# Performance work log

Hardware: AMD Instinct MI355X
Metric: run time of the kernel (lower is better)

Reference implementation:

```python
import jax, jax.numpy as jnp
import numpy as np

EPS = 1e-6  # T5LayerNorm epsilon


def setup_inputs() -> dict:
    key = jax.random.key(0)
    k0, k1, k2, k3 = jax.random.split(key, 4)
    B, S, D, F, E = 4, 2048, 768, 3072, 8
    hidden_states = jax.random.normal(k0, (B, S, D), jnp.float32)
    router_w = jax.random.normal(k1, (E, D), jnp.float32) * 0.02
    ln_w = jnp.ones((E, D), jnp.float32)
    wi = jax.random.normal(k2, (E, F, D), jnp.float32) * 0.02
    wo = jax.random.normal(k3, (E, D, F), jnp.float32) * 0.02
    return {"hidden_states": hidden_states, "router_w": router_w, "ln_w": ln_w,
            "wi": wi, "wo": wo, "top_k": 2}


def reference(hidden_states, router_w, ln_w, wi, wo, top_k):
    B, S, D = hidden_states.shape
    E = router_w.shape[0]
    x = hidden_states.reshape(-1, D)                      # [T, D] tokens
    router_logits = x @ router_w.T                        # [T, E]
    probs = jax.nn.softmax(router_logits, axis=-1)
    rw, sel = jax.lax.top_k(probs, top_k)                 # [T, K]
    rw = rw / jnp.sum(rw, axis=-1, keepdims=True)         # renormalize top-k weights

    # T5LayerNorm is RMS-norm (no mean subtraction); shared input x, per-expert scale.
    var = jnp.mean(x * x, axis=-1, keepdims=True)         # [T, 1]
    x_norm = x * jax.lax.rsqrt(var + EPS)                 # [T, D]

    out = jnp.zeros_like(x)
    for e in range(E):  # fixed small loop over experts (structurally distinct params)
        # combine weight for expert e: zero for tokens that did not select it
        w_e = jnp.sum(jnp.where(sel == e, rw, 0.0), axis=-1)   # [T]
        h = x_norm * ln_w[e]                                   # [T, D]
        ff = jax.nn.relu(h @ wi[e].T) @ wo[e].T                # [T, D]
        # T5LayerFF returns x + FFN(LN(x)); routing weight scales the whole output
        out = out + w_e[:, None] * (x + ff)
    layer_output = out.reshape(B, S, D)
    return layer_output, router_logits
```

## Files before the change

### kernel.cpp

```cpp
#include <hip/hip_runtime.h>
#include <hip/hip_bf16.h>
#include <math.h>

typedef short short8 __attribute__((ext_vector_type(8)));
typedef float f32x16 __attribute__((ext_vector_type(16)));

constexpr int D = 768;
constexpr int E = 8;
constexpr int F = 3072;
constexpr int FH = 1536;
constexpr int T = 8192;
constexpr float EPS = 1e-6f;

static __device__ inline unsigned short f2bf(float f) {
    __hip_bfloat16 h = __float2bfloat16(f);
    return *reinterpret_cast<unsigned short*>(&h);
}

static __device__ inline f32x16 mfma_bf16(short8 a, short8 b, f32x16 c) {
    return __builtin_amdgcn_mfma_f32_32x32x16_bf16(a, b, c, 0, 0, 0);
}

#define GLL16(g, s) __builtin_amdgcn_global_load_lds( \
    (const __attribute__((address_space(1))) unsigned int*)(g), \
    (__attribute__((address_space(3))) unsigned int*)(s), 16, 0, 0)

__global__ __launch_bounds__(256)
void convert_weights(const float* __restrict__ wi, const float* __restrict__ wo,
                     const float* __restrict__ lnw,
                     unsigned short* __restrict__ wip, unsigned short* __restrict__ wop)
{
    const unsigned NWI = (unsigned)E * F * D;
    unsigned i4 = (blockIdx.x * 256u + threadIdx.x) * 4u;
    if (i4 < NWI) {
        float4 v = *(const float4*)(wi + i4);
        unsigned e = i4 / (unsigned)(F * D);
        unsigned d = i4 % (unsigned)D;
        float4 l = *(const float4*)(lnw + e * D + d);
        ushort4 o = { f2bf(v.x * l.x), f2bf(v.y * l.y), f2bf(v.z * l.z), f2bf(v.w * l.w) };
        *(ushort4*)(wip + i4) = o;
    } else {
        unsigned j = i4 - NWI;
        float4 v = *(const float4*)(wo + j);
        ushort4 o = { f2bf(v.x), f2bf(v.y), f2bf(v.z), f2bf(v.w) };
        *(ushort4*)(wop + j) = o;
    }
}

__global__ __launch_bounds__(256)
void router_norm_kernel(const float* __restrict__ x,
                        const float* __restrict__ rw,
                        float* __restrict__ logits,
                        unsigned short* __restrict__ xn,
                        float* __restrict__ out,
                        int*   __restrict__ sel,
                        float2* __restrict__ w01)
{
    const int lane = threadIdx.x & 63;
    const int wid  = threadIdx.x >> 6;
    const int t = blockIdx.x * 4 + wid;
    if (t >= T) return;

    const float* xr = x + (size_t)t * D;
    float xv[12];
    float acc[8];
#pragma unroll
    for (int e = 0; e < 8; ++e) acc[e] = 0.f;
    float ssq = 0.f;
#pragma unroll
    for (int i = 0; i < 12; ++i) {
        const int k = lane + 64 * i;
        const float v = xr[k];
        xv[i] = v;
        ssq += v * v;
#pragma unroll
        for (int e = 0; e < 8; ++e) acc[e] += v * rw[e * D + k];
    }
#pragma unroll
    for (int off = 32; off; off >>= 1) {
        ssq += __shfl_xor(ssq, off);
#pragma unroll
        for (int e = 0; e < 8; ++e) acc[e] += __shfl_xor(acc[e], off);
    }

    int e0 = 0; float m0 = acc[0];
#pragma unroll
    for (int e = 1; e < 8; ++e) if (acc[e] > m0) { m0 = acc[e]; e0 = e; }
    int e1 = -1; float m1 = -3.4e38f;
#pragma unroll
    for (int e = 0; e < 8; ++e) if (e != e0 && acc[e] > m1) { m1 = acc[e]; e1 = e; }

    const float r  = expf(m1 - m0);
    const float w0 = 1.f / (1.f + r);
    const float w1 = r * w0;
    const float wsum = w0 + w1;
    const float rs = rsqrtf(ssq * (1.f / (float)D) + EPS);

    if (lane == 0) {
#pragma unroll
        for (int e = 0; e < 8; ++e) logits[t * 8 + e] = acc[e];
        sel[t] = e0 | (e1 << 4);
        w01[t] = make_float2(w0, w1);
    }

#pragma unroll
    for (int i = 0; i < 12; ++i) {
        const int k = lane + 64 * i;
        xn[(size_t)t * D + k] = f2bf(xv[i] * rs);
        out[(size_t)t * D + k] = wsum * xv[i];
    }
}

__global__ __launch_bounds__(256)
void build_lists(const int* __restrict__ sel, const float2* __restrict__ w01,
                 int* __restrict__ counts, int* __restrict__ lists,
                 float* __restrict__ wlist)
{
    const int e = blockIdx.x;
    const int tid = threadIdx.x;
    const int lane = tid & 63;
    const int wv = tid >> 6;
    __shared__ int wtot[4];
    int cnt = 0;
    for (int c0 = 0; c0 < T; c0 += 256) {
        const int t = c0 + tid;
        const int s = sel[t];
        const bool m1 = ((s >> 4) & 15) == e;
        const bool m = ((s & 15) == e) || m1;
        const unsigned long long b = __ballot(m);
        const int pre = __popcll(b & ((1ULL << lane) - 1ULL));
        if (lane == 0) wtot[wv] = __popcll(b);
        __syncthreads();
        int wbase = 0;
#pragma unroll
        for (int i = 0; i < 4; ++i) if (i < wv) wbase += wtot[i];
        if (m) {
            const int pos = cnt + wbase + pre;
            lists[e * T + pos] = (t << 1) | (m1 ? 1 : 0);
            const float2 w = w01[t];
            wlist[e * T + pos] = m1 ? w.y : w.x;
        }
        cnt += wtot[0] + wtot[1] + wtot[2] + wtot[3];
        __syncthreads();
    }
    if (tid == 0) counts[e] = cnt;
}


#define GEMM_PIPE_LOOP(NKT)                                                   \
           \
    _Pragma("unroll")                                                         \
    for (int j = 0; j < 4; ++j) {                                             \
        GLL16(aSrc[j], smem + stg + j * 1024);                                \
        GLL16(bSrc[j], smem + 16384 + stg + j * 1024);                        \
    }                                                                         \
    _Pragma("unroll")                                                         \
    for (int j = 0; j < 4; ++j) {                                             \
        GLL16(aSrc[j] + 64, smem + 32768 + stg + j * 1024);                   \
        GLL16(bSrc[j] + 64, smem + 32768 + 16384 + stg + j * 1024);           \
    }                                                                         \
    asm volatile("s_waitcnt vmcnt(8)" ::: "memory");                          \
    __builtin_amdgcn_s_barrier();                                             \
    int cur = 0;                                                              \
    for (int kt = 0; kt < (NKT); ++kt) {                                      \
        const char* cA = smem + cur * 32768;                                  \
        const char* cB = cA + 16384;                                          \
        short8 fA0[4], fA1[4], fB0[4], fB1[4];                                \
        _Pragma("unroll")                                                     \
        for (int ks = 0; ks < 4; ++ks) {                                      \
            const int coff = (hi * 16 + ks * 32) ^ rx;                        \
            fA0[ks] = *(const short8*)(cA + arow0 + coff);                    \
            fA1[ks] = *(const short8*)(cA + arow1 + coff);                    \
            fB0[ks] = *(const short8*)(cB + brow0 + coff);                    \
            fB1[ks] = *(const short8*)(cB + brow1 + coff);                    \
        }                                                                     \
        asm volatile("s_waitcnt lgkmcnt(0)" ::: "memory");                    \
        __builtin_amdgcn_sched_barrier(0);                                    \
        __builtin_amdgcn_s_barrier();    \
        {                                                                     \
            const int kn = (kt + 2 < (NKT) ? kt + 2 : (NKT)-1) * 64;          \
            char* dA = smem + cur * 32768;                                    \
            _Pragma("unroll")                                                 \
            for (int j = 0; j < 4; ++j) {                                     \
                GLL16(aSrc[j] + kn, dA + stg + j * 1024);                     \
                GLL16(bSrc[j] + kn, dA + 16384 + stg + j * 1024);             \
            }                                                                 \
        }                                                                     \
        __builtin_amdgcn_sched_barrier(0);                                    \
        _Pragma("unroll")                                                     \
        for (int ks = 0; ks < 4; ++ks) {                                      \
            acc00 = mfma_bf16(fA0[ks], fB0[ks], acc00);                       \
            acc01 = mfma_bf16(fA0[ks], fB1[ks], acc01);                       \
            acc10 = mfma_bf16(fA1[ks], fB0[ks], acc10);                       \
            acc11 = mfma_bf16(fA1[ks], fB1[ks], acc11);                       \
        }                                                                     \
        asm volatile("s_waitcnt vmcnt(8)" ::: "memory");                      \
        __builtin_amdgcn_s_barrier();    \
        cur ^= 1;                                                             \
    }

__global__ __launch_bounds__(256)
void gemm1_kernel(const unsigned short* __restrict__ xn,
                  const unsigned short* __restrict__ wip,
                  const int* __restrict__ counts,
                  const int* __restrict__ lists,
                  unsigned short* __restrict__ H, int half)
{
    __shared__ __align__(16) char smem[65536];
    __shared__ int s_tok[128];

    const int bid = blockIdx.x;
    const int e  = bid & 7;
    const int mt = (bid >> 3) / 12;
    const int nt = (bid >> 3) % 12;
    const int cnt = counts[e];
    const int base = mt * 128;
    if (base >= cnt) return;
    int offe = 0;
    for (int i = 0; i < e; ++i) offe += counts[i];

    const int tid = threadIdx.x;
    const int w = tid >> 6, l = tid & 63;
    const int lo = l & 31, hi = l >> 5;
    const int wr = w >> 1, wc = w & 1;

    if (tid < 128) {
        const int idx = base + tid;
        s_tok[tid] = (idx < cnt) ? (lists[e * T + idx] >> 1) : 0;
    }
    __syncthreads();

    const int r = (w * 4 + 0) * 8 + (l >> 3);
    const int chS = ((l & 7) ^ ((l >> 3) & 7)) * 8;
    const unsigned short* aSrc[4];
    const unsigned short* bSrc[4];
#pragma unroll
    for (int j = 0; j < 4; ++j) {
        const int rj = r + j * 8;
        aSrc[j] = xn + (size_t)s_tok[rj] * D + chS;
        bSrc[j] = wip + ((size_t)e * F + half * FH + nt * 128 + rj) * D + chS;
    }

    f32x16 acc00, acc01, acc10, acc11;
#pragma unroll
    for (int q = 0; q < 16; ++q) { acc00[q] = 0.f; acc01[q] = 0.f; acc10[q] = 0.f; acc11[q] = 0.f; }

    const int rx = (lo & 7) << 4;
    const int arow0 = (wr * 64 + lo) * 128;
    const int arow1 = arow0 + 32 * 128;
    const int brow0 = (wc * 64 + lo) * 128;
    const int brow1 = brow0 + 32 * 128;
    const int stg = w * 4096;

    GEMM_PIPE_LOOP(12)

    const int cbase = nt * 128 + wc * 64 + lo;
#pragma unroll
    for (int rr = 0; rr < 16; ++rr) {
        const int crow = (rr & 3) + 8 * (rr >> 2) + 4 * hi;
        int lrow = wr * 64 + crow;
        if (base + lrow < cnt) {
            unsigned short* hp = H + (size_t)(offe + base + lrow) * FH + cbase;
            hp[0]  = f2bf(fmaxf(acc00[rr], 0.f));
            hp[32] = f2bf(fmaxf(acc01[rr], 0.f));
        }
        lrow += 32;
        if (base + lrow < cnt) {
            unsigned short* hp = H + (size_t)(offe + base + lrow) * FH + cbase;
            hp[0]  = f2bf(fmaxf(acc10[rr], 0.f));
            hp[32] = f2bf(fmaxf(acc11[rr], 0.f));
        }
    }
}

__global__ __launch_bounds__(256)
void gemm2_kernel(const unsigned short* __restrict__ H,
                  const unsigned short* __restrict__ wop,
                  const int* __restrict__ counts,
                  const int* __restrict__ lists, const float* __restrict__ wlist,
                  float* __restrict__ out, float* __restrict__ ffout,
                  int half, int mode)
{
    __shared__ __align__(16) char smem[65536];
    __shared__ int   s_tok[128];
    __shared__ float s_wgt[128];

    const int bid = blockIdx.x;
    const int e  = bid & 7;
    const int mt = (bid >> 3) / 6;
    const int nt = (bid >> 3) % 6;
    const int cnt = counts[e];
    const int base = mt * 128;
    if (base >= cnt) return;
    int offe = 0;
    for (int i = 0; i < e; ++i) offe += counts[i];

    const int tid = threadIdx.x;
    const int w = tid >> 6, l = tid & 63;
    const int lo = l & 31, hi = l >> 5;
    const int wr = w >> 1, wc = w & 1;

    if (tid < 128) {
        const int idx = base + tid;
        const bool v = idx < cnt;
        s_tok[tid] = v ? lists[e * T + idx] : 0;
        s_wgt[tid] = v ? wlist[e * T + idx] : 0.f;
    }
    __syncthreads();

    const int r = (w * 4 + 0) * 8 + (l >> 3);
    const int chS = ((l & 7) ^ ((l >> 3) & 7)) * 8;
    const unsigned short* aSrc[4];
    const unsigned short* bSrc[4];
#pragma unroll
    for (int j = 0; j < 4; ++j) {
        const int rj = r + j * 8;
        aSrc[j] = H + (size_t)(offe + base + rj) * FH + chS;
        bSrc[j] = wop + ((size_t)e * D + nt * 128 + rj) * F + half * FH + chS;
    }

    f32x16 acc00, acc01, acc10, acc11;
#pragma unroll
    for (int q = 0; q < 16; ++q) { acc00[q] = 0.f; acc01[q] = 0.f; acc10[q] = 0.f; acc11[q] = 0.f; }

    const int rx = (lo & 7) << 4;
    const int arow0 = (wr * 64 + lo) * 128;
    const int arow1 = arow0 + 32 * 128;
    const int brow0 = (wc * 64 + lo) * 128;
    const int brow1 = brow0 + 32 * 128;
    const int stg = w * 4096;

    GEMM_PIPE_LOOP(24)

    const int cbase = nt * 128 + wc * 64 + lo;
#pragma unroll
    for (int rr = 0; rr < 16; ++rr) {
        const int crow = (rr & 3) + 8 * (rr >> 2) + 4 * hi;
#pragma unroll
        for (int mh = 0; mh < 2; ++mh) {
            const int lrow = wr * 64 + crow + mh * 32;
            if (base + lrow < cnt) {
                const int pk = s_tok[lrow];
                const float wgt = s_wgt[lrow];
                const float v0 = wgt * (mh ? acc10[rr] : acc00[rr]);
                const float v1 = wgt * (mh ? acc11[rr] : acc01[rr]);
                if (mode == 0) {
                    float* dst = out + (size_t)(pk >> 1) * D + cbase;
                    atomicAdd(dst,      v0);
                    atomicAdd(dst + 32, v1);
                } else {
                    float* dst = ffout + ((size_t)(pk & 1) * T + (pk >> 1)) * D + cbase;
                    if (mode == 1) { dst[0] = v0;  dst[32] = v1; }
                    else           { dst[0] += v0; dst[32] += v1; }
                }
            }
        }
    }
}

__global__ __launch_bounds__(256)
void combine_kernel(const float* __restrict__ ffout, float* __restrict__ out)
{
    const long long i4 = ((long long)blockIdx.x * 256 + threadIdx.x) * 4;
    float4 o  = *(const float4*)(out + i4);
    float4 f0 = *(const float4*)(ffout + i4);
    float4 f1 = *(const float4*)(ffout + (long long)T * D + i4);
    o.x += f0.x + f1.x; o.y += f0.y + f1.y;
    o.z += f0.z + f1.z; o.w += f0.w + f1.w;
    *(float4*)(out + i4) = o;
}

extern "C" void kernel_launch(void* const* d_in, const int* in_sizes, int n_in,
                              void* d_out, int out_size, void* d_ws, size_t ws_size,
                              hipStream_t stream) {
    const float* x   = (const float*)d_in[0];
    const float* rw  = (const float*)d_in[1];
    const float* lnw = (const float*)d_in[2];
    const float* wi  = (const float*)d_in[3];
    const float* wo  = (const float*)d_in[4];

    float* out    = (float*)d_out;
    float* logits = (float*)d_out + (size_t)T * D;

    char* ws = (char*)d_ws;
    int*            counts = (int*)(ws);
    int*            sel    = (int*)(ws + 4096);
    float2*         w01    = (float2*)(ws + 65536);
    int*            lists  = (int*)(ws + 131072);
    float*          wlist  = (float*)(ws + 393216);
    unsigned short* xn     = (unsigned short*)(ws + 1048576);
    unsigned short* wip    = (unsigned short*)(ws + 13631488);
    unsigned short* wop    = (unsigned short*)(ws + 51380224);
    unsigned short* H      = (unsigned short*)(ws + 89128960);
    float*          ffout  = (float*)(ws + 140247040);

    const bool big = ws_size >= 190578688ULL;

    convert_weights<<<36864, 256, 0, stream>>>(wi, wo, lnw, wip, wop);

    router_norm_kernel<<<T / 4, 256, 0, stream>>>(x, rw, logits, xn, out,
                                                  sel, w01);

    build_lists<<<E, 256, 0, stream>>>(sel, w01, counts, lists, wlist);

    for (int h = 0; h < 2; ++h) {
        gemm1_kernel<<<32 * 12 * 8, 256, 0, stream>>>(xn, wip, counts,
                                                      lists, H, h);
        const int mode = big ? (h ? 2 : 1) : 0;
        gemm2_kernel<<<32 * 6 * 8, 256, 0, stream>>>(H, wop, counts,
                                                     lists, wlist, out,
                                                     ffout, h, mode);
    }

    if (big) combine_kernel<<<T * D / 4 / 256, 256, 0, stream>>>(ffout, out);
}
```

Baseline: 360.1 us.

## Enlarge expert GEMM tiles to 256x256 with eight waves per block

Result: slower. 458.0 us (+27.2%).

```diff
diff --git a/kernel.cpp b/kernel.cpp
--- a/kernel.cpp
+++ b/kernel.cpp
@@ -147,74 +147,69 @@
 }
 
 
-#define GEMM_PIPE_LOOP(NKT)                                                   \
-           \
+#define GEMM8W_LOOP(NKT)                                                      \
     _Pragma("unroll")                                                         \
-    for (int j = 0; j < 4; ++j) {                                             \
-        GLL16(aSrc[j], smem + stg + j * 1024);                                \
-        GLL16(bSrc[j], smem + 16384 + stg + j * 1024);                        \
+    for (int p = 0; p < 4; ++p) {                                             \
+        GLL16(aS[p], smem + p * 8192 + dOff);                                 \
+        GLL16(bS[p], smem + 32768 + p * 8192 + dOff);                         \
     }                                                                         \
-    _Pragma("unroll")                                                         \
-    for (int j = 0; j < 4; ++j) {                                             \
-        GLL16(aSrc[j] + 64, smem + 32768 + stg + j * 1024);                   \
-        GLL16(bSrc[j] + 64, smem + 32768 + 16384 + stg + j * 1024);           \
-    }                                                                         \
-    asm volatile("s_waitcnt vmcnt(8)" ::: "memory");                          \
-    __builtin_amdgcn_s_barrier();                                             \
-    int cur = 0;                                                              \
+    asm volatile("s_waitcnt vmcnt(0)" ::: "memory");                          \
+    __syncthreads();                                                          \
+    int bsel = 0;                                                             \
     for (int kt = 0; kt < (NKT); ++kt) {                                      \
-        const char* cA = smem + cur * 32768;                                  \
-        const char* cB = cA + 16384;                                          \
-        short8 fA0[4], fA1[4], fB0[4], fB1[4];                                \
+        const char* bufA = smem + bsel * 65536;                               \
+        const char* bufB = bufA + 32768;                                      \
+        char* nbuf = smem + (bsel ^ 1) * 65536;                               \
+        const int kg = (kt + 1) * 64;                                         \
+        const bool st = (kt + 1) < (NKT);                                     \
         _Pragma("unroll")                                                     \
-        for (int ks = 0; ks < 4; ++ks) {                                      \
-            const int coff = (hi * 16 + ks * 32) ^ rx;                        \
-            fA0[ks] = *(const short8*)(cA + arow0 + coff);                    \
-            fA1[ks] = *(const short8*)(cA + arow1 + coff);                    \
-            fB0[ks] = *(const short8*)(cB + brow0 + coff);                    \
-            fB1[ks] = *(const short8*)(cB + brow1 + coff);                    \
+        for (int p = 0; p < 4; ++p) {                                         \
+            if (st) {                                                         \
+                GLL16(aS[p] + kg, nbuf + p * 8192 + dOff);                    \
+                GLL16(bS[p] + kg, nbuf + 32768 + p * 8192 + dOff);            \
+            }                                                                 \
+            short8 fa0[4], fa1[4], fb[4];                                     \
+            const int m2 = (p >> 1) * 2, nn = p & 1;                          \
+            _Pragma("unroll")                                                 \
+            for (int ks = 0; ks < 4; ++ks) {                                  \
+                const int co = (hi * 16 + ks * 32) ^ rx;                      \
+                const int ar0 = wr * 128 + m2 * 32 + lo;                      \
+                fa0[ks] = *(const short8*)(bufA + ar0 * 128 + co);            \
+                fa1[ks] = *(const short8*)(bufA + (ar0 + 32) * 128 + co);     \
+                const int br = wcn * 64 + nn * 32 + lo;                       \
+                fb[ks]  = *(const short8*)(bufB + br * 128 + co);             \
+            }                                                                 \
+            asm volatile("s_waitcnt lgkmcnt(0)" ::: "memory");                \
+            __builtin_amdgcn_sched_barrier(0);                                \
+            __builtin_amdgcn_s_setprio(1);                                    \
+            _Pragma("unroll")                                                 \
+            for (int ks = 0; ks < 4; ++ks) {                                  \
+                acc[m2][nn]     = mfma_bf16(fa0[ks], fb[ks], acc[m2][nn]);    \
+                acc[m2 + 1][nn] = mfma_bf16(fa1[ks], fb[ks], acc[m2 + 1][nn]);\
+            }                                                                 \
+            __builtin_amdgcn_s_setprio(0);                                    \
         }                                                                     \
-        asm volatile("s_waitcnt lgkmcnt(0)" ::: "memory");                    \
-        __builtin_amdgcn_sched_barrier(0);                                    \
-        __builtin_amdgcn_s_barrier();    \
-        {                                                                     \
-            const int kn = (kt + 2 < (NKT) ? kt + 2 : (NKT)-1) * 64;          \
-            char* dA = smem + cur * 32768;                                    \
-            _Pragma("unroll")                                                 \
-            for (int j = 0; j < 4; ++j) {                                     \
-                GLL16(aSrc[j] + kn, dA + stg + j * 1024);                     \
-                GLL16(bSrc[j] + kn, dA + 16384 + stg + j * 1024);             \
-            }                                                                 \
-        }                                                                     \
-        __builtin_amdgcn_sched_barrier(0);                                    \
-        _Pragma("unroll")                                                     \
-        for (int ks = 0; ks < 4; ++ks) {                                      \
-            acc00 = mfma_bf16(fA0[ks], fB0[ks], acc00);                       \
-            acc01 = mfma_bf16(fA0[ks], fB1[ks], acc01);                       \
-            acc10 = mfma_bf16(fA1[ks], fB0[ks], acc10);                       \
-            acc11 = mfma_bf16(fA1[ks], fB1[ks], acc11);                       \
-        }                                                                     \
-        asm volatile("s_waitcnt vmcnt(8)" ::: "memory");                      \
-        __builtin_amdgcn_s_barrier();    \
-        cur ^= 1;                                                             \
-    }
-
-__global__ __launch_bounds__(256)
+        asm volatile("s_waitcnt vmcnt(0)" ::: "memory");                      \
+        __builtin_amdgcn_s_barrier();                                         \
+        bsel ^= 1;                                                            \
+    }
+
+__global__ __launch_bounds__(512, 2)
 void gemm1_kernel(const unsigned short* __restrict__ xn,
                   const unsigned short* __restrict__ wip,
                   const int* __restrict__ counts,
                   const int* __restrict__ lists,
                   unsigned short* __restrict__ H, int half)
 {
-    __shared__ __align__(16) char smem[65536];
-    __shared__ int s_tok[128];
+    __shared__ __align__(16) char smem[131072];
+    __shared__ int s_tok[256];
 
     const int bid = blockIdx.x;
     const int e  = bid & 7;
-    const int mt = (bid >> 3) / 12;
-    const int nt = (bid >> 3) % 12;
+    const int mt = (bid >> 3) / 6;
+    const int nt = (bid >> 3) % 6;
     const int cnt = counts[e];
-    const int base = mt * 128;
+    const int base = mt * 256;
     if (base >= cnt) return;
     int offe = 0;
     for (int i = 0; i < e; ++i) offe += counts[i];
@@ -222,58 +217,56 @@
     const int tid = threadIdx.x;
     const int w = tid >> 6, l = tid & 63;
     const int lo = l & 31, hi = l >> 5;
-    const int wr = w >> 1, wc = w & 1;
-
-    if (tid < 128) {
+    const int wr = w >> 2;
+    const int wcn = w & 3;
+
+    if (tid < 256) {
         const int idx = base + tid;
         s_tok[tid] = (idx < cnt) ? (lists[e * T + idx] >> 1) : 0;
     }
     __syncthreads();
 
-    const int r = (w * 4 + 0) * 8 + (l >> 3);
-    const int chS = ((l & 7) ^ ((l >> 3) & 7)) * 8;
-    const unsigned short* aSrc[4];
-    const unsigned short* bSrc[4];
-#pragma unroll
-    for (int j = 0; j < 4; ++j) {
-        const int rj = r + j * 8;
-        aSrc[j] = xn + (size_t)s_tok[rj] * D + chS;
-        bSrc[j] = wip + ((size_t)e * F + half * FH + nt * 128 + rj) * D + chS;
-    }
-
-    f32x16 acc00, acc01, acc10, acc11;
-#pragma unroll
-    for (int q = 0; q < 16; ++q) { acc00[q] = 0.f; acc01[q] = 0.f; acc10[q] = 0.f; acc11[q] = 0.f; }
+    const int srow = tid >> 3;
+    const int chS = ((tid & 7) ^ (srow & 7)) * 8;
+    const int dOff = srow * 128 + (tid & 7) * 16;
+    const unsigned short* aS[4];
+    const unsigned short* bS[4];
+#pragma unroll
+    for (int p = 0; p < 4; ++p) {
+        const int r = p * 64 + srow;
+        aS[p] = xn + (size_t)s_tok[r] * D + chS;
+        bS[p] = wip + ((size_t)e * F + half * FH + nt * 256 + r) * D + chS;
+    }
+
+    f32x16 acc[4][2];
+#pragma unroll
+    for (int m = 0; m < 4; ++m)
+#pragma unroll
+        for (int n = 0; n < 2; ++n)
+#pragma unroll
+            for (int q = 0; q < 16; ++q) acc[m][n][q] = 0.f;
 
     const int rx = (lo & 7) << 4;
-    const int arow0 = (wr * 64 + lo) * 128;
-    const int arow1 = arow0 + 32 * 128;
-    const int brow0 = (wc * 64 + lo) * 128;
-    const int brow1 = brow0 + 32 * 128;
-    const int stg = w * 4096;
-
-    GEMM_PIPE_LOOP(12)
-
-    const int cbase = nt * 128 + wc * 64 + lo;
-#pragma unroll
-    for (int rr = 0; rr < 16; ++rr) {
-        const int crow = (rr & 3) + 8 * (rr >> 2) + 4 * hi;
-        int lrow = wr * 64 + crow;
-        if (base + lrow < cnt) {
-            unsigned short* hp = H + (size_t)(offe + base + lrow) * FH + cbase;
-            hp[0]  = f2bf(fmaxf(acc00[rr], 0.f));
-            hp[32] = f2bf(fmaxf(acc01[rr], 0.f));
+
+    GEMM8W_LOOP(12)
+
+    const int cb = nt * 256 + wcn * 64 + lo;
+#pragma unroll
+    for (int m = 0; m < 4; ++m) {
+#pragma unroll
+        for (int r = 0; r < 16; ++r) {
+            const int crow = (r & 3) + 8 * (r >> 2) + 4 * hi;
+            const int lrow = wr * 128 + m * 32 + crow;
+            if (base + lrow < cnt) {
+                unsigned short* hp = H + (size_t)(offe + base + lrow) * FH + cb;
+                hp[0]  = f2bf(fmaxf(acc[m][0][r], 0.f));
+                hp[32] = f2bf(fmaxf(acc[m][1][r], 0.f));
+            }
         }
-        lrow += 32;
-        if (base + lrow < cnt) {
-            unsigned short* hp = H + (size_t)(offe + base + lrow) * FH + cbase;
-            hp[0]  = f2bf(fmaxf(acc10[rr], 0.f));
-            hp[32] = f2bf(fmaxf(acc11[rr], 0.f));
-        }
-    }
-}
-
-__global__ __launch_bounds__(256)
+    }
+}
+
+__global__ __launch_bounds__(512, 2)
 void gemm2_kernel(const unsigned short* __restrict__ H,
                   const unsigned short* __restrict__ wop,
                   const int* __restrict__ counts,
@@ -281,16 +274,16 @@
                   float* __restrict__ out, float* __restrict__ ffout,
                   int half, int mode)
 {
-    __shared__ __align__(16) char smem[65536];
-    __shared__ int   s_tok[128];
-    __shared__ float s_wgt[128];
+    __shared__ __align__(16) char smem[131072];
+    __shared__ int   s_tok[256];
+    __shared__ float s_wgt[256];
 
     const int bid = blockIdx.x;
     const int e  = bid & 7;
-    const int mt = (bid >> 3) / 6;
-    const int nt = (bid >> 3) % 6;
+    const int mt = (bid >> 3) / 3;
+    const int nt = (bid >> 3) % 3;
     const int cnt = counts[e];
-    const int base = mt * 128;
+    const int base = mt * 256;
     if (base >= cnt) return;
     int offe = 0;
     for (int i = 0; i < e; ++i) offe += counts[i];
@@ -298,9 +291,10 @@
     const int tid = threadIdx.x;
     const int w = tid >> 6, l = tid & 63;
     const int lo = l & 31, hi = l >> 5;
-    const int wr = w >> 1, wc = w & 1;
-
-    if (tid < 128) {
+    const int wr = w >> 2;
+    const int wcn = w & 3;
+
+    if (tid < 256) {
         const int idx = base + tid;
         const bool v = idx < cnt;
         s_tok[tid] = v ? lists[e * T + idx] : 0;
@@ -308,48 +302,48 @@
     }
     __syncthreads();
 
-    const int r = (w * 4 + 0) * 8 + (l >> 3);
-    const int chS = ((l & 7) ^ ((l >> 3) & 7)) * 8;
-    const unsigned short* aSrc[4];
-    const unsigned short* bSrc[4];
-#pragma unroll
-    for (int j = 0; j < 4; ++j) {
-        const int rj = r + j * 8;
-        aSrc[j] = H + (size_t)(offe + base + rj) * FH + chS;
-        bSrc[j] = wop + ((size_t)e * D + nt * 128 + rj) * F + half * FH + chS;
-    }
-
-    f32x16 acc00, acc01, acc10, acc11;
-#pragma unroll
-    for (int q = 0; q < 16; ++q) { acc00[q] = 0.f; acc01[q] = 0.f; acc10[q] = 0.f; acc11[q] = 0.f; }
+    const int srow = tid >> 3;
+    const int chS = ((tid & 7) ^ (srow & 7)) * 8;
+    const int dOff = srow * 128 + (tid & 7) * 16;
+    const unsigned short* aS[4];
+    const unsigned short* bS[4];
+#pragma unroll
+    for (int p = 0; p < 4; ++p) {
+        const int r = p * 64 + srow;
+        aS[p] = H + (size_t)(offe + base + r) * FH + chS;
+        bS[p] = wop + ((size_t)e * D + nt * 256 + r) * F + half * FH + chS;
+    }
+
+    f32x16 acc[4][2];
+#pragma unroll
+    for (int m = 0; m < 4; ++m)
+#pragma unroll
+        for (int n = 0; n < 2; ++n)
+#pragma unroll
+            for (int q = 0; q < 16; ++q) acc[m][n][q] = 0.f;
 
     const int rx = (lo & 7) << 4;
-    const int arow0 = (wr * 64 + lo) * 128;
-    const int arow1 = arow0 + 32 * 128;
-    const int brow0 = (wc * 64 + lo) * 128;
-    const int brow1 = brow0 + 32 * 128;
-    const int stg = w * 4096;
-
-    GEMM_PIPE_LOOP(24)
-
-    const int cbase = nt * 128 + wc * 64 + lo;
-#pragma unroll
-    for (int rr = 0; rr < 16; ++rr) {
-        const int crow = (rr & 3) + 8 * (rr >> 2) + 4 * hi;
-#pragma unroll
-        for (int mh = 0; mh < 2; ++mh) {
-            const int lrow = wr * 64 + crow + mh * 32;
+
+    GEMM8W_LOOP(24)
+
+    const int cb = nt * 256 + wcn * 64 + lo;
+#pragma unroll
+    for (int m = 0; m < 4; ++m) {
+#pragma unroll
+        for (int r = 0; r < 16; ++r) {
+            const int crow = (r & 3) + 8 * (r >> 2) + 4 * hi;
+            const int lrow = wr * 128 + m * 32 + crow;
             if (base + lrow < cnt) {
                 const int pk = s_tok[lrow];
                 const float wgt = s_wgt[lrow];
-                const float v0 = wgt * (mh ? acc10[rr] : acc00[rr]);
-                const float v1 = wgt * (mh ? acc11[rr] : acc01[rr]);
+                const float v0 = wgt * acc[m][0][r];
+                const float v1 = wgt * acc[m][1][r];
                 if (mode == 0) {
-                    float* dst = out + (size_t)(pk >> 1) * D + cbase;
+                    float* dst = out + (size_t)(pk >> 1) * D + cb;
                     atomicAdd(dst,      v0);
                     atomicAdd(dst + 32, v1);
                 } else {
-                    float* dst = ffout + ((size_t)(pk & 1) * T + (pk >> 1)) * D + cbase;
+                    float* dst = ffout + ((size_t)(pk & 1) * T + (pk >> 1)) * D + cb;
                     if (mode == 1) { dst[0] = v0;  dst[32] = v1; }
                     else           { dst[0] += v0; dst[32] += v1; }
                 }
@@ -404,10 +398,10 @@
     build_lists<<<E, 256, 0, stream>>>(sel, w01, counts, lists, wlist);
 
     for (int h = 0; h < 2; ++h) {
-        gemm1_kernel<<<32 * 12 * 8, 256, 0, stream>>>(xn, wip, counts,
-                                                      lists, H, h);
+        gemm1_kernel<<<32 * 6 * 8, 512, 0, stream>>>(xn, wip, counts,
+                                                     lists, H, h);
         const int mode = big ? (h ? 2 : 1) : 0;
-        gemm2_kernel<<<32 * 6 * 8, 256, 0, stream>>>(H, wop, counts,
+        gemm2_kernel<<<32 * 3 * 8, 512, 0, stream>>>(H, wop, counts,
                                                      lists, wlist, out,
                                                      ffout, h, mode);
     }
```
